# Performance work log

Hardware: AMD Instinct MI355X
Metric: run time of the kernel (lower is better)

## Reference

```python
import jax, jax.numpy as jnp
import numpy as np

B = 1024      # graphs
NODES = 128   # nodes per graph (uniform -> batch_ptr = arange(B+1)*NODES)
IN = 64
HID = 256
OUT = 128
NBLK = 3
TAU = 0.25


def _ln(x, g, b):
    # LayerNorm over last dim, eps=1e-5 (torch default)
    mu = jnp.mean(x, axis=-1, keepdims=True)
    var = jnp.mean((x - mu) ** 2, axis=-1, keepdims=True)
    return (x - mu) / jnp.sqrt(var + 1e-5) * g + b


def setup_inputs() -> dict:
    key = jax.random.key(0)
    ks = jax.random.split(key, 4)
    sc = 0.05
    return {
        "H": jax.random.normal(ks[0], (B * NODES, IN), jnp.float32),
        "batch_ptr": jnp.arange(B + 1, dtype=jnp.int32) * NODES,
        # ResNetMLP params: stem Linear(IN->HID)+LN, NBLK residual blocks
        # Linear(HID->HID)+LN+ReLU, head Linear(HID->OUT)+LN (last_norm=True).
        "W_in": jax.random.normal(ks[1], (IN, HID), jnp.float32) * sc,
        "b_in": jnp.zeros((HID,), jnp.float32),
        "g_in": jnp.ones((HID,), jnp.float32),
        "beta_in": jnp.zeros((HID,), jnp.float32),
        "Wb": jax.random.normal(ks[2], (NBLK, HID, HID), jnp.float32) * sc,
        "bb": jnp.zeros((NBLK, HID), jnp.float32),
        "gb": jnp.ones((NBLK, HID), jnp.float32),
        "betab": jnp.zeros((NBLK, HID), jnp.float32),
        "W_out": jax.random.normal(ks[3], (HID, OUT), jnp.float32) * sc,
        "b_out": jnp.zeros((OUT,), jnp.float32),
        "g_out": jnp.ones((OUT,), jnp.float32),
        "beta_out": jnp.zeros((OUT,), jnp.float32),
    }


def reference(H, batch_ptr, W_in, b_in, g_in, beta_in, Wb, bb, gb, betab,
              W_out, b_out, g_out, beta_out):
    # ResNetMLP projection (dropout is identity in eval)
    x = jax.nn.relu(_ln(H @ W_in + b_in, g_in, beta_in))          # [N, HID]
    for k in range(NBLK):
        x = x + jax.nn.relu(_ln(x @ Wb[k] + bb[k], gb[k], betab[k]))
    z = _ln(x @ W_out + b_out, g_out, beta_out)                   # [N, OUT]

    # Uniform-size graphs: ragged per-graph loop vectorizes to [Bg, n, OUT]
    Bg = batch_ptr.shape[0] - 1
    n = H.shape[0] // Bg
    z3 = z.reshape(Bg, n, OUT)

    # s_i = mean_j ||z_i - z_j||_2 (includes j=i, distance 0)
    sq = jnp.sum(z3 * z3, axis=-1)                                # [Bg, n]
    d2 = sq[:, :, None] + sq[:, None, :] - 2.0 * jnp.einsum("bid,bjd->bij", z3, z3)
    d = jnp.sqrt(jnp.maximum(d2, 0.0) + 1e-12)                    # [Bg, n, n]
    s = jnp.mean(d, axis=-1)                                      # [Bg, n]

    w = jax.nn.softmax(s / TAU, axis=-1)                          # [Bg, n]
    v_loc = jnp.einsum("bi,bid->bd", w, z3)                       # [Bg, OUT]
    return v_loc, w
```

## Files before the change

kernel.cpp:

```cpp
#include <hip/hip_runtime.h>
#include <stdint.h>


typedef __attribute__((ext_vector_type(8))) short bf16x8;
typedef __attribute__((ext_vector_type(4))) float f32x4;

#define XB_STRIDE 264
#define YB_STRIDE 260
#define ZB_STRIDE 136
#define LDS_PAR   66560
#define LDS_TOTAL 69632

__device__ __forceinline__ unsigned int rne16(float f) {
  unsigned int u = __builtin_bit_cast(unsigned int, f);
  return u + 0x7fffu + ((u >> 16) & 1u);
}
__device__ __forceinline__ unsigned short f2bf(float f) {
  return (unsigned short)(rne16(f) >> 16);
}
__device__ __forceinline__ float bf2f(unsigned short h) {
  unsigned int u = ((unsigned int)h) << 16;
  return __builtin_bit_cast(float, u);
}
__device__ __forceinline__ f32x4 zero4() {
  f32x4 v; v.x = 0.f; v.y = 0.f; v.z = 0.f; v.w = 0.f; return v;
}
template <int CTRL>
__device__ __forceinline__ float dpp_add(float v) {
  int p = __builtin_amdgcn_update_dpp(0, __builtin_bit_cast(int, v),
                                      CTRL, 0xF, 0xF, true);
  return v + __builtin_bit_cast(float, p);
}
__device__ __forceinline__ float red16(float v) {
  v = dpp_add<0xB1>(v);
  v = dpp_add<0x4E>(v);
  v = dpp_add<0x141>(v);
  v = dpp_add<0x140>(v);
  return v;
}

__global__ void prep_weights(const float* __restrict__ Win, const float* __restrict__ Wb,
                             const float* __restrict__ Wout, unsigned short* __restrict__ ws) {
  int g = blockIdx.x * 256 + threadIdx.x;
  if (g >= 30720) return;
  const float* W; int N; int local;
  if (g < 2048) { W = Win; N = 256; local = g; }
  else if (g < 26624) {
    int i = g - 2048; int blk = i >> 13; local = i & 8191;
    W = Wb + blk * 65536; N = 256;
  } else { W = Wout; N = 128; local = g - 26624; }
  int f = local >> 6, lane = local & 63;
  int NTL = N >> 4;
  int kc = f / NTL, ntile = f - kc * NTL;
  int n = ntile * 16 + (lane & 15);
  int k0 = kc * 32 + (lane >> 4) * 8;
  unsigned short o[8];
#pragma unroll
  for (int e = 0; e < 8; ++e) o[e] = f2bf(W[(size_t)(k0 + e) * N + n]);
  *reinterpret_cast<uint4*>(ws + (size_t)g * 8) = *reinterpret_cast<uint4*>(o);
}

template <int KL, int N, int MODE>
__device__ __forceinline__ void layer(unsigned short* __restrict__ Xb,
                                      float* __restrict__ Yb, float* __restrict__ par,
                                      const unsigned short* __restrict__ Wf,
                                      int tid, int wave, int lane,
                                      const float* __restrict__ bias,
                                      const float* __restrict__ gam,
                                      const float* __restrict__ bet,
                                      float (&xprev)[32],
                                      unsigned short* __restrict__ Z, size_t rowglob) {
  constexpr int NT = N / 128;
  constexpr int NTL = N / 16;
  constexpr int KC = KL / 32;
  constexpr int J = N / 64;
  const int wc = wave;
  const int q = lane >> 4, l16 = lane & 15;
  const int colbase = wc * 16 * NT;
  const unsigned short* Wl = Wf + lane * 8;

  f32x4 acc[4][NT];
#pragma unroll
  for (int mt = 0; mt < 4; ++mt)
#pragma unroll
    for (int nt = 0; nt < NT; ++nt) acc[mt][nt] = zero4();

  bf16x8 bcur[NT];
#pragma unroll
  for (int nt = 0; nt < NT; ++nt)
    bcur[nt] = *reinterpret_cast<const bf16x8*>(Wl + (size_t)(wc * NT + nt) * 512);

  __syncthreads();
  for (int t = tid; t < 3 * N; t += 512) {
    float v = (t < N) ? bias[t] : (t < 2 * N) ? gam[t - N] : bet[t - 2 * N];
    par[t] = v;
  }
#pragma unroll
  for (int kc = 0; kc < KC; ++kc) {
    bf16x8 bnext[NT];
    if (kc + 1 < KC) {
#pragma unroll
      for (int nt = 0; nt < NT; ++nt)
        bnext[nt] = *reinterpret_cast<const bf16x8*>(
            Wl + (size_t)((kc + 1) * NTL + wc * NT + nt) * 512);
    }
    const int kk = kc * 32 + q * 8;
#pragma unroll
    for (int mt = 0; mt < 4; ++mt) {
      bf16x8 a = *reinterpret_cast<const bf16x8*>(Xb + (16 * mt + l16) * XB_STRIDE + kk);
#pragma unroll
      for (int nt = 0; nt < NT; ++nt)
        acc[mt][nt] = __builtin_amdgcn_mfma_f32_16x16x32_bf16(a, bcur[nt], acc[mt][nt], 0, 0, 0);
    }
    if (kc + 1 < KC) {
#pragma unroll
      for (int nt = 0; nt < NT; ++nt) bcur[nt] = bnext[nt];
    }
  }

  __syncthreads();

#pragma unroll
  for (int mt = 0; mt < 4; ++mt)
#pragma unroll
    for (int nt = 0; nt < NT; ++nt) {
      const int col = colbase + 16 * nt + l16;
#pragma unroll
      for (int r = 0; r < 4; ++r)
        Yb[(16 * mt + 4 * q + r) * YB_STRIDE + col] = acc[mt][nt][r];
    }
  __syncthreads();

  const int cb = l16 * 4;
  unsigned int pk[2][2 * J];
#pragma unroll
  for (int h = 0; h < 2; ++h) {
    const int row = 32 * h + wave * 4 + q;
    float s1 = 0.f, s2 = 0.f;
#pragma unroll
    for (int j = 0; j < J; ++j) {
      f32x4 yv = *reinterpret_cast<const f32x4*>(Yb + row * YB_STRIDE + cb + 64 * j);
      f32x4 bv = *reinterpret_cast<const f32x4*>(par + cb + 64 * j);
#pragma unroll
      for (int i = 0; i < 4; ++i) {
        float t = yv[i] + bv[i];
        s1 += t; s2 = __builtin_fmaf(t, t, s2);
      }
    }
    s1 = red16(s1); s2 = red16(s2);
    const float mu = s1 * (1.0f / N);
    const float var = s2 * (1.0f / N) - mu * mu;
    const float rstd = rsqrtf(var + 1e-5f);
    const float nmr = -mu * rstd;
#pragma unroll
    for (int j = 0; j < J; ++j) {
      f32x4 yv = *reinterpret_cast<const f32x4*>(Yb + row * YB_STRIDE + cb + 64 * j);
      f32x4 bv = *reinterpret_cast<const f32x4*>(par + cb + 64 * j);
      f32x4 gv = *reinterpret_cast<const f32x4*>(par + N + cb + 64 * j);
      f32x4 ev = *reinterpret_cast<const f32x4*>(par + 2 * N + cb + 64 * j);
#pragma unroll
      for (int i = 0; i < 4; ++i) {
        const int e = 16 * h + 4 * j + i;
        float t = __builtin_fmaf(yv[i] + bv[i], rstd, nmr);
        float o = __builtin_fmaf(t, gv[i], ev[i]);
        float xv;
        if constexpr (MODE == 0) { xv = fmaxf(o, 0.f); xprev[e] = xv; }
        else if constexpr (MODE == 1) { xv = xprev[e] + fmaxf(o, 0.f); xprev[e] = xv; }
        else { xv = o; (void)e; }
        if (i & 1)
          pk[h][2 * j + (i >> 1)] = __builtin_amdgcn_perm(rne16(xv),
                         rne16(__builtin_bit_cast(float, pk[h][2 * j + (i >> 1)])), 0x07060302);
        else
          pk[h][2 * j + (i >> 1)] = __builtin_bit_cast(unsigned int, xv);
      }
    }
    if constexpr (MODE == 2) {
#pragma unroll
      for (int j = 0; j < J; ++j)
        *reinterpret_cast<uint2*>(Z + (rowglob + row) * 128 + cb + 64 * j) =
            *reinterpret_cast<uint2*>(&pk[h][2 * j]);
    }
  }
  if constexpr (MODE != 2) {
    __syncthreads();
    unsigned int* Xw = reinterpret_cast<unsigned int*>(Xb);
#pragma unroll
    for (int h = 0; h < 2; ++h) {
      const int row = 32 * h + wave * 4 + q;
#pragma unroll
      for (int j = 0; j < J; ++j)
        *reinterpret_cast<uint2*>(Xw + row * 132 + 2 * l16 + 32 * j) =
            *reinterpret_cast<uint2*>(&pk[h][2 * j]);
    }
  }
}

__global__ __attribute__((amdgpu_flat_work_group_size(512, 512), amdgpu_waves_per_eu(4)))
void mlp_main(const float* __restrict__ H, const unsigned short* __restrict__ ws,
              const float* __restrict__ b_in, const float* __restrict__ g_in,
              const float* __restrict__ beta_in,
              const float* __restrict__ bb, const float* __restrict__ gb,
              const float* __restrict__ betab,
              const float* __restrict__ b_out, const float* __restrict__ g_out,
              const float* __restrict__ beta_out,
              unsigned short* __restrict__ Z) {
  extern __shared__ char smem[];
  unsigned short* Xb = (unsigned short*)smem;
  float* Yb = (float*)smem;
  float* par = (float*)(smem + LDS_PAR);
  const int tid = threadIdx.x;
  const int wave = tid >> 6, lane = tid & 63;
  const size_t rowglob = (size_t)blockIdx.x * 64;

  {
    int row = tid >> 3, c8 = (tid & 7) * 8;
    const float* hp = H + (rowglob + row) * 64 + c8;
    float4 f0 = *reinterpret_cast<const float4*>(hp);
    float4 f1 = *reinterpret_cast<const float4*>(hp + 4);
    uint4 o;
    o.x = __builtin_amdgcn_perm(rne16(f0.y), rne16(f0.x), 0x07060302);
    o.y = __builtin_amdgcn_perm(rne16(f0.w), rne16(f0.z), 0x07060302);
    o.z = __builtin_amdgcn_perm(rne16(f1.y), rne16(f1.x), 0x07060302);
    o.w = __builtin_amdgcn_perm(rne16(f1.w), rne16(f1.z), 0x07060302);
    *reinterpret_cast<uint4*>(Xb + row * XB_STRIDE + c8) = o;
  }

  float xprev[32];
  layer<64, 256, 0>(Xb, Yb, par, ws,           tid, wave, lane, b_in,     g_in,     beta_in,     xprev, Z, rowglob);
  layer<256, 256, 1>(Xb, Yb, par, ws + 16384,  tid, wave, lane, bb,       gb,       betab,       xprev, Z, rowglob);
  layer<256, 256, 1>(Xb, Yb, par, ws + 81920,  tid, wave, lane, bb + 256, gb + 256, betab + 256, xprev, Z, rowglob);
  layer<256, 256, 1>(Xb, Yb, par, ws + 147456, tid, wave, lane, bb + 512, gb + 512, betab + 512, xprev, Z, rowglob);
  layer<256, 128, 2>(Xb, Yb, par, ws + 212992, tid, wave, lane, b_out,    g_out,    beta_out,    xprev, Z, rowglob);
}

__global__ __attribute__((amdgpu_flat_work_group_size(512, 512)))
void pool_main(const unsigned short* __restrict__ Z, float* __restrict__ out) {
  __shared__ unsigned short Zb[128 * ZB_STRIDE];
  __shared__ float sqv[128], sm[128], smw[128];
  const int tid = threadIdx.x;
  const int g = blockIdx.x;
  const int wave = tid >> 6, lane = tid & 63;
  const int q = lane >> 4, l16 = lane & 15;

  {
    int zr = tid >> 2, zc = (tid & 3) * 32;
    const uint4* zp = reinterpret_cast<const uint4*>(Z + ((size_t)g * 128 + zr) * 128 + zc);
    uint4* zd = reinterpret_cast<uint4*>(Zb + zr * ZB_STRIDE + zc);
    zd[0] = zp[0]; zd[1] = zp[1]; zd[2] = zp[2]; zd[3] = zp[3];
  }
  __syncthreads();

  f32x4 g2[8];
#pragma unroll
  for (int nt = 0; nt < 8; ++nt) g2[nt] = zero4();
#pragma unroll
  for (int ks = 0; ks < 4; ++ks) {
    int kk = ks * 32 + q * 8;
    bf16x8 a = *reinterpret_cast<const bf16x8*>(Zb + (16 * wave + l16) * ZB_STRIDE + kk);
#pragma unroll
    for (int nt = 0; nt < 8; ++nt) {
      bf16x8 bfr = *reinterpret_cast<const bf16x8*>(Zb + (16 * nt + l16) * ZB_STRIDE + kk);
      g2[nt] = __builtin_amdgcn_mfma_f32_16x16x32_bf16(a, bfr, g2[nt], 0, 0, 0);
    }
  }
  if ((l16 >> 2) == q) {
#pragma unroll
    for (int nt = 0; nt < 8; ++nt)
      if (nt == wave) {
#pragma unroll
        for (int r = 0; r < 4; ++r)
          if ((l16 & 3) == r) sqv[16 * wave + l16] = g2[nt][r];
      }
  }
  __syncthreads();
  float sqi[4];
#pragma unroll
  for (int r = 0; r < 4; ++r) sqi[r] = sqv[16 * wave + q * 4 + r];
  float sp[4] = {0.f, 0.f, 0.f, 0.f};
#pragma unroll
  for (int nt = 0; nt < 8; ++nt) {
    float sqj = sqv[16 * nt + l16];
#pragma unroll
    for (int r = 0; r < 4; ++r) {
      float d2 = sqi[r] + sqj - 2.0f * g2[nt][r];
      sp[r] += sqrtf(fmaxf(d2, 0.f) + 1e-12f);
    }
  }
#pragma unroll
  for (int d = 1; d < 16; d <<= 1) {
#pragma unroll
    for (int r = 0; r < 4; ++r) { float t = sp[r]; t += __shfl_xor(t, d); sp[r] = t; }
  }
  if (l16 == 0) {
#pragma unroll
    for (int r = 0; r < 4; ++r) sm[16 * wave + q * 4 + r] = sp[r] * (1.0f / 128.0f);
  }
  __syncthreads();
  if (wave == 0) {
    float l0 = sm[lane] * 4.0f;
    float l1 = sm[lane + 64] * 4.0f;
    float mx = fmaxf(l0, l1);
#pragma unroll
    for (int d = 1; d < 64; d <<= 1) mx = fmaxf(mx, __shfl_xor(mx, d));
    float e0 = __expf(l0 - mx), e1 = __expf(l1 - mx);
    float ss = e0 + e1;
#pragma unroll
    for (int d = 1; d < 64; d <<= 1) ss += __shfl_xor(ss, d);
    float inv = 1.0f / ss;
    float w0 = e0 * inv, w1 = e1 * inv;
    smw[lane] = w0;
    smw[lane + 64] = w1;
    out[131072 + g * 128 + lane] = w0;
    out[131072 + g * 128 + 64 + lane] = w1;
  }
  __syncthreads();
  {
    int c = 16 * wave + l16;
    float acv = 0.f;
#pragma unroll
    for (int i0 = 0; i0 < 32; ++i0) {
      int i = q * 32 + i0;
      acv += smw[i] * bf2f(Zb[i * ZB_STRIDE + c]);
    }
    acv += __shfl_xor(acv, 16);
    acv += __shfl_xor(acv, 32);
    if (q == 0) out[g * 128 + c] = acv;
  }
}

extern "C" void kernel_launch(void* const* d_in, const int* in_sizes, int n_in,
                              void* d_out, int out_size, void* d_ws, size_t ws_size,
                              hipStream_t stream) {
  (void)in_sizes; (void)n_in; (void)out_size; (void)ws_size;
  const float* H        = (const float*)d_in[0];
  const float* W_in     = (const float*)d_in[2];
  const float* b_in     = (const float*)d_in[3];
  const float* g_in     = (const float*)d_in[4];
  const float* beta_in  = (const float*)d_in[5];
  const float* Wb       = (const float*)d_in[6];
  const float* bb       = (const float*)d_in[7];
  const float* gb       = (const float*)d_in[8];
  const float* betab    = (const float*)d_in[9];
  const float* W_out    = (const float*)d_in[10];
  const float* b_out    = (const float*)d_in[11];
  const float* g_out    = (const float*)d_in[12];
  const float* beta_out = (const float*)d_in[13];
  float* out = (float*)d_out;
  unsigned short* ws = (unsigned short*)d_ws;
  unsigned short* Z = ws + 262144;

  prep_weights<<<120, 256, 0, stream>>>(W_in, Wb, W_out, ws);
  hipFuncSetAttribute(reinterpret_cast<const void*>(mlp_main),
                      hipFuncAttributeMaxDynamicSharedMemorySize, LDS_TOTAL);
  mlp_main<<<2048, 512, LDS_TOTAL, stream>>>(H, ws, b_in, g_in, beta_in,
                                             bb, gb, betab, b_out, g_out, beta_out, Z);
  pool_main<<<1024, 512, 0, stream>>>(Z, out);
}
```

Measured before the change: 209.7 us.

## Fuse MLP and per-graph pooling into one 1024-thread kernel per graph

Merges the MLP kernel and the pooling kernel so that each 1024-thread block processes a whole 128-node graph. The final Z tile stays in LDS instead of being written to global memory and read back, and one kernel launch is removed. The cost is a much larger LDS footprint (about 134 KB per block), so only one block fits per CU. During the pooling stage half of the 16 waves sit idle, and every block waits on extra barriers.

```diff
diff --git a/kernel.cpp b/kernel.cpp
--- a/kernel.cpp
+++ b/kernel.cpp
@@ -8,8 +8,9 @@
 #define XB_STRIDE 264
 #define YB_STRIDE 260
 #define ZB_STRIDE 136
-#define LDS_PAR   66560
-#define LDS_TOTAL 69632
+#define LDS_PAR   133120
+#define LDS_SQV   136192
+#define LDS_TOTAL 137728
 
 __device__ __forceinline__ unsigned int rne16(float f) {
   unsigned int u = __builtin_bit_cast(unsigned int, f);
@@ -68,14 +69,14 @@
                                       const float* __restrict__ bias,
                                       const float* __restrict__ gam,
                                       const float* __restrict__ bet,
-                                      float (&xprev)[32],
-                                      unsigned short* __restrict__ Z, size_t rowglob) {
+                                      float (&xprev)[32]) {
   constexpr int NT = N / 128;
   constexpr int NTL = N / 16;
   constexpr int KC = KL / 32;
   constexpr int J = N / 64;
-  const int wc = wave;
+  const int wr = wave >> 3, wc = wave & 7;
   const int q = lane >> 4, l16 = lane & 15;
+  const int rbase = 64 * wr;
   const int colbase = wc * 16 * NT;
   const unsigned short* Wl = Wf + lane * 8;
 
@@ -91,7 +92,7 @@
     bcur[nt] = *reinterpret_cast<const bf16x8*>(Wl + (size_t)(wc * NT + nt) * 512);
 
   __syncthreads();
-  for (int t = tid; t < 3 * N; t += 512) {
+  for (int t = tid; t < 3 * N; t += 1024) {
     float v = (t < N) ? bias[t] : (t < 2 * N) ? gam[t - N] : bet[t - 2 * N];
     par[t] = v;
   }
@@ -107,7 +108,7 @@
     const int kk = kc * 32 + q * 8;
 #pragma unroll
     for (int mt = 0; mt < 4; ++mt) {
-      bf16x8 a = *reinterpret_cast<const bf16x8*>(Xb + (16 * mt + l16) * XB_STRIDE + kk);
+      bf16x8 a = *reinterpret_cast<const bf16x8*>(Xb + (rbase + 16 * mt + l16) * XB_STRIDE + kk);
 #pragma unroll
       for (int nt = 0; nt < NT; ++nt)
         acc[mt][nt] = __builtin_amdgcn_mfma_f32_16x16x32_bf16(a, bcur[nt], acc[mt][nt], 0, 0, 0);
@@ -127,7 +128,7 @@
       const int col = colbase + 16 * nt + l16;
 #pragma unroll
       for (int r = 0; r < 4; ++r)
-        Yb[(16 * mt + 4 * q + r) * YB_STRIDE + col] = acc[mt][nt][r];
+        Yb[(rbase + 16 * mt + 4 * q + r) * YB_STRIDE + col] = acc[mt][nt][r];
     }
   __syncthreads();
 
@@ -135,7 +136,7 @@
   unsigned int pk[2][2 * J];
 #pragma unroll
   for (int h = 0; h < 2; ++h) {
-    const int row = 32 * h + wave * 4 + q;
+    const int row = 64 * h + 4 * wave + q;
     float s1 = 0.f, s2 = 0.f;
 #pragma unroll
     for (int j = 0; j < J; ++j) {
@@ -174,28 +175,32 @@
           pk[h][2 * j + (i >> 1)] = __builtin_bit_cast(unsigned int, xv);
       }
     }
-    if constexpr (MODE == 2) {
-#pragma unroll
-      for (int j = 0; j < J; ++j)
-        *reinterpret_cast<uint2*>(Z + (rowglob + row) * 128 + cb + 64 * j) =
-            *reinterpret_cast<uint2*>(&pk[h][2 * j]);
-    }
-  }
+  }
+  __syncthreads();
   if constexpr (MODE != 2) {
-    __syncthreads();
     unsigned int* Xw = reinterpret_cast<unsigned int*>(Xb);
 #pragma unroll
     for (int h = 0; h < 2; ++h) {
-      const int row = 32 * h + wave * 4 + q;
+      const int row = 64 * h + 4 * wave + q;
 #pragma unroll
       for (int j = 0; j < J; ++j)
         *reinterpret_cast<uint2*>(Xw + row * 132 + 2 * l16 + 32 * j) =
             *reinterpret_cast<uint2*>(&pk[h][2 * j]);
     }
-  }
-}
-
-__global__ __attribute__((amdgpu_flat_work_group_size(512, 512), amdgpu_waves_per_eu(4)))
+  } else {
+    unsigned short* Zb = Xb;
+#pragma unroll
+    for (int h = 0; h < 2; ++h) {
+      const int row = 64 * h + 4 * wave + q;
+#pragma unroll
+      for (int j = 0; j < J; ++j)
+        *reinterpret_cast<uint2*>(Zb + row * ZB_STRIDE + cb + 64 * j) =
+            *reinterpret_cast<uint2*>(&pk[h][2 * j]);
+    }
+  }
+}
+
+__global__ __attribute__((amdgpu_flat_work_group_size(1024, 1024), amdgpu_waves_per_eu(4)))
 void mlp_main(const float* __restrict__ H, const unsigned short* __restrict__ ws,
               const float* __restrict__ b_in, const float* __restrict__ g_in,
               const float* __restrict__ beta_in,
@@ -203,14 +208,18 @@
               const float* __restrict__ betab,
               const float* __restrict__ b_out, const float* __restrict__ g_out,
               const float* __restrict__ beta_out,
-              unsigned short* __restrict__ Z) {
+              float* __restrict__ out) {
   extern __shared__ char smem[];
   unsigned short* Xb = (unsigned short*)smem;
   float* Yb = (float*)smem;
   float* par = (float*)(smem + LDS_PAR);
+  float* sqv = (float*)(smem + LDS_SQV);
+  float* sm = sqv + 128;
+  float* smw = sm + 128;
   const int tid = threadIdx.x;
   const int wave = tid >> 6, lane = tid & 63;
-  const size_t rowglob = (size_t)blockIdx.x * 64;
+  const int g = blockIdx.x;
+  const size_t rowglob = (size_t)g * 128;
 
   {
     int row = tid >> 3, c8 = (tid & 7) * 8;
@@ -226,74 +235,64 @@
   }
 
   float xprev[32];
-  layer<64, 256, 0>(Xb, Yb, par, ws,           tid, wave, lane, b_in,     g_in,     beta_in,     xprev, Z, rowglob);
-  layer<256, 256, 1>(Xb, Yb, par, ws + 16384,  tid, wave, lane, bb,       gb,       betab,       xprev, Z, rowglob);
-  layer<256, 256, 1>(Xb, Yb, par, ws + 81920,  tid, wave, lane, bb + 256, gb + 256, betab + 256, xprev, Z, rowglob);
-  layer<256, 256, 1>(Xb, Yb, par, ws + 147456, tid, wave, lane, bb + 512, gb + 512, betab + 512, xprev, Z, rowglob);
-  layer<256, 128, 2>(Xb, Yb, par, ws + 212992, tid, wave, lane, b_out,    g_out,    beta_out,    xprev, Z, rowglob);
-}
-
-__global__ __attribute__((amdgpu_flat_work_group_size(512, 512)))
-void pool_main(const unsigned short* __restrict__ Z, float* __restrict__ out) {
-  __shared__ unsigned short Zb[128 * ZB_STRIDE];
-  __shared__ float sqv[128], sm[128], smw[128];
-  const int tid = threadIdx.x;
-  const int g = blockIdx.x;
-  const int wave = tid >> 6, lane = tid & 63;
+  layer<64, 256, 0>(Xb, Yb, par, ws,           tid, wave, lane, b_in,     g_in,     beta_in,     xprev);
+  layer<256, 256, 1>(Xb, Yb, par, ws + 16384,  tid, wave, lane, bb,       gb,       betab,       xprev);
+  layer<256, 256, 1>(Xb, Yb, par, ws + 81920,  tid, wave, lane, bb + 256, gb + 256, betab + 256, xprev);
+  layer<256, 256, 1>(Xb, Yb, par, ws + 147456, tid, wave, lane, bb + 512, gb + 512, betab + 512, xprev);
+  layer<256, 128, 2>(Xb, Yb, par, ws + 212992, tid, wave, lane, b_out,    g_out,    beta_out,    xprev);
+
+  unsigned short* Zb = Xb;
   const int q = lane >> 4, l16 = lane & 15;
-
-  {
-    int zr = tid >> 2, zc = (tid & 3) * 32;
-    const uint4* zp = reinterpret_cast<const uint4*>(Z + ((size_t)g * 128 + zr) * 128 + zc);
-    uint4* zd = reinterpret_cast<uint4*>(Zb + zr * ZB_STRIDE + zc);
-    zd[0] = zp[0]; zd[1] = zp[1]; zd[2] = zp[2]; zd[3] = zp[3];
-  }
   __syncthreads();
 
   f32x4 g2[8];
-#pragma unroll
-  for (int nt = 0; nt < 8; ++nt) g2[nt] = zero4();
-#pragma unroll
-  for (int ks = 0; ks < 4; ++ks) {
-    int kk = ks * 32 + q * 8;
-    bf16x8 a = *reinterpret_cast<const bf16x8*>(Zb + (16 * wave + l16) * ZB_STRIDE + kk);
+  if (wave < 8) {
+#pragma unroll
+    for (int nt = 0; nt < 8; ++nt) g2[nt] = zero4();
+#pragma unroll
+    for (int ks = 0; ks < 4; ++ks) {
+      int kk = ks * 32 + q * 8;
+      bf16x8 a = *reinterpret_cast<const bf16x8*>(Zb + (16 * wave + l16) * ZB_STRIDE + kk);
+#pragma unroll
+      for (int nt = 0; nt < 8; ++nt) {
+        bf16x8 bfr = *reinterpret_cast<const bf16x8*>(Zb + (16 * nt + l16) * ZB_STRIDE + kk);
+        g2[nt] = __builtin_amdgcn_mfma_f32_16x16x32_bf16(a, bfr, g2[nt], 0, 0, 0);
+      }
+    }
+    if ((l16 >> 2) == q) {
+#pragma unroll
+      for (int nt = 0; nt < 8; ++nt)
+        if (nt == wave) {
+#pragma unroll
+          for (int r = 0; r < 4; ++r)
+            if ((l16 & 3) == r) sqv[16 * wave + l16] = g2[nt][r];
+        }
+    }
+  }
+  __syncthreads();
+  if (wave < 8) {
+    float sqi[4];
+#pragma unroll
+    for (int r = 0; r < 4; ++r) sqi[r] = sqv[16 * wave + q * 4 + r];
+    float sp[4] = {0.f, 0.f, 0.f, 0.f};
 #pragma unroll
     for (int nt = 0; nt < 8; ++nt) {
-      bf16x8 bfr = *reinterpret_cast<const bf16x8*>(Zb + (16 * nt + l16) * ZB_STRIDE + kk);
-      g2[nt] = __builtin_amdgcn_mfma_f32_16x16x32_bf16(a, bfr, g2[nt], 0, 0, 0);
-    }
-  }
-  if ((l16 >> 2) == q) {
-#pragma unroll
-    for (int nt = 0; nt < 8; ++nt)
-      if (nt == wave) {
-#pragma unroll
-        for (int r = 0; r < 4; ++r)
-          if ((l16 & 3) == r) sqv[16 * wave + l16] = g2[nt][r];
+      float sqj = sqv[16 * nt + l16];
+#pragma unroll
+      for (int r = 0; r < 4; ++r) {
+        float d2 = sqi[r] + sqj - 2.0f * g2[nt][r];
+        sp[r] += sqrtf(fmaxf(d2, 0.f) + 1e-12f);
       }
-  }
-  __syncthreads();
-  float sqi[4];
-#pragma unroll
-  for (int r = 0; r < 4; ++r) sqi[r] = sqv[16 * wave + q * 4 + r];
-  float sp[4] = {0.f, 0.f, 0.f, 0.f};
-#pragma unroll
-  for (int nt = 0; nt < 8; ++nt) {
-    float sqj = sqv[16 * nt + l16];
-#pragma unroll
-    for (int r = 0; r < 4; ++r) {
-      float d2 = sqi[r] + sqj - 2.0f * g2[nt][r];
-      sp[r] += sqrtf(fmaxf(d2, 0.f) + 1e-12f);
-    }
-  }
-#pragma unroll
-  for (int d = 1; d < 16; d <<= 1) {
-#pragma unroll
-    for (int r = 0; r < 4; ++r) { float t = sp[r]; t += __shfl_xor(t, d); sp[r] = t; }
-  }
-  if (l16 == 0) {
-#pragma unroll
-    for (int r = 0; r < 4; ++r) sm[16 * wave + q * 4 + r] = sp[r] * (1.0f / 128.0f);
+    }
+#pragma unroll
+    for (int d = 1; d < 16; d <<= 1) {
+#pragma unroll
+      for (int r = 0; r < 4; ++r) { float t = sp[r]; t += __shfl_xor(t, d); sp[r] = t; }
+    }
+    if (l16 == 0) {
+#pragma unroll
+      for (int r = 0; r < 4; ++r) sm[16 * wave + q * 4 + r] = sp[r] * (1.0f / 128.0f);
+    }
   }
   __syncthreads();
   if (wave == 0) {
@@ -314,7 +313,7 @@
     out[131072 + g * 128 + 64 + lane] = w1;
   }
   __syncthreads();
-  {
+  if (wave < 8) {
     int c = 16 * wave + l16;
     float acv = 0.f;
 #pragma unroll
@@ -347,12 +346,10 @@
   const float* beta_out = (const float*)d_in[13];
   float* out = (float*)d_out;
   unsigned short* ws = (unsigned short*)d_ws;
-  unsigned short* Z = ws + 262144;
 
   prep_weights<<<120, 256, 0, stream>>>(W_in, Wb, W_out, ws);
   hipFuncSetAttribute(reinterpret_cast<const void*>(mlp_main),
                       hipFuncAttributeMaxDynamicSharedMemorySize, LDS_TOTAL);
-  mlp_main<<<2048, 512, LDS_TOTAL, stream>>>(H, ws, b_in, g_in, beta_in,
-                                             bb, gb, betab, b_out, g_out, beta_out, Z);
-  pool_main<<<1024, 512, 0, stream>>>(Z, out);
-}
+  mlp_main<<<1024, 1024, LDS_TOTAL, stream>>>(H, ws, b_in, g_in, beta_in,
+                                              bb, gb, betab, b_out, g_out, beta_out, out);
+}
```

Measured after the change: 228.0 us. +8.7%, slower.
